# Kernel optimization log

Hardware: AMD Instinct MI355X
Metric: run time of the kernel (lower is better)

The kernel has to match this reference:

```python
import jax, jax.numpy as jnp
import numpy as np

Q = 1024   # num_queries = 32*32
S = 1024   # memory / out seq len
B = 8      # batch
D = 256    # hidden_dim
H = 8      # nhead
FF = 1024  # dim_feedforward (expert hidden)
E = 8      # moe_nume
K = 2      # moe_topk
EPS = 1e-5


def layer_norm(x, g, b):
    mu = jnp.mean(x, axis=-1, keepdims=True)
    var = jnp.var(x, axis=-1, keepdims=True)
    return (x - mu) * jax.lax.rsqrt(var + EPS) * g + b


def mha(q, k, v, wi, bi, wo, bo):
    # q: [Lq,B,D], k/v: [Lk,B,D]; torch nn.MultiheadAttention math (packed in_proj)
    Lq, Bq, Dm = q.shape
    Lk = k.shape[0]
    hd = Dm // H
    wq, wk, wv = jnp.split(wi, 3, axis=0)
    bq, bk, bv = jnp.split(bi, 3)
    qp = (q @ wq.T + bq).reshape(Lq, Bq, H, hd).transpose(1, 2, 0, 3)  # [B,H,Lq,hd]
    kp = (k @ wk.T + bk).reshape(Lk, Bq, H, hd).transpose(1, 2, 0, 3)  # [B,H,Lk,hd]
    vp = (v @ wv.T + bv).reshape(Lk, Bq, H, hd).transpose(1, 2, 0, 3)
    scores = jnp.einsum('bhqd,bhkd->bhqk', qp, kp) / jnp.sqrt(jnp.asarray(hd, q.dtype))
    attn = jax.nn.softmax(scores, axis=-1)
    o = jnp.einsum('bhqk,bhkd->bhqd', attn, vp)          # [B,H,Lq,hd]
    o = o.transpose(2, 0, 1, 3).reshape(Lq, Bq, Dm)       # back to [Lq,B,D]
    return o @ wo.T + bo


def moe_ffn(x, gate_w, gate_b, w1, b1, w2, b2):
    # x: [T,D]. NaiveGate: top-k of linear logits, softmax over the k logits.
    logits = x @ gate_w.T + gate_b                        # [T,E]
    vals, idx = jax.lax.top_k(logits, K)                  # [T,K]
    score = jax.nn.softmax(vals, axis=-1)                 # [T,K]
    T = x.shape[0]
    g = jnp.zeros((T, E), x.dtype).at[jnp.arange(T)[:, None], idx].set(score)
    y = jnp.zeros_like(x)
    for e in range(E):  # fixed small expert count
        h = jax.nn.relu(x @ w1[e].T + b1[e])              # [T,FF]
        y = y + g[:, e:e + 1] * (h @ w2[e].T + b2[e])     # [T,D]
    return y


def setup_inputs() -> dict:
    key = jax.random.key(0)
    ks = jax.random.split(key, 24)
    sc = 0.02
    n = lambda i, shp, s=sc: jax.random.normal(ks[i], shp, jnp.float32) * s
    return {
        'out':    jax.random.normal(ks[0], (S, B, D), jnp.float32),
        'memory': jax.random.normal(ks[1], (S, B, D), jnp.float32),
        'embed':  jax.random.normal(ks[2], (Q, D), jnp.float32),
        'sa_wi': n(3, (3 * D, D)), 'sa_bi': jnp.zeros((3 * D,), jnp.float32),
        'sa_wo': n(4, (D, D)),     'sa_bo': jnp.zeros((D,), jnp.float32),
        'ca_wi': n(5, (3 * D, D)), 'ca_bi': jnp.zeros((3 * D,), jnp.float32),
        'ca_wo': n(6, (D, D)),     'ca_bo': jnp.zeros((D,), jnp.float32),
        'n1_g': jnp.ones((D,), jnp.float32), 'n1_b': jnp.zeros((D,), jnp.float32),
        'n2_g': jnp.ones((D,), jnp.float32), 'n2_b': jnp.zeros((D,), jnp.float32),
        'gate_w': n(7, (E, D)), 'gate_b': jnp.zeros((E,), jnp.float32),
        'w1': n(8, (E, FF, D)), 'b1': jnp.zeros((E, FF), jnp.float32),
        'w2': n(9, (E, D, FF)), 'b2': jnp.zeros((E, D), jnp.float32),
    }


def reference(out, memory, embed, sa_wi, sa_bi, sa_wo, sa_bo,
              ca_wi, ca_bi, ca_wo, ca_bo, n1_g, n1_b, n2_g, n2_b,
              gate_w, gate_b, w1, b1, w2, b2):
    # forward_post path (normalize_before=False); pos/masks are None; dropout=eval
    tgt = jnp.broadcast_to(embed[:, None, :], (Q, B, D))
    t2 = mha(tgt, memory, memory, sa_wi, sa_bi, sa_wo, sa_bo)
    tgt = layer_norm(tgt + t2, n1_g, n1_b)
    t2 = mha(tgt, out, out, ca_wi, ca_bi, ca_wo, ca_bo)
    tgt = layer_norm(tgt + t2, n2_g, n2_b)
    # CustomizedMoEPositionwiseFF, pre_lnorm=False: output = inp + moe(inp)
    core = moe_ffn(tgt.reshape(-1, D), gate_w, gate_b, w1, b1, w2, b2).reshape(Q, B, D)
    return tgt + core
```

## Files before the change

### kernel.cpp

```cpp
#include <hip/hip_runtime.h>
#include <hip/hip_bf16.h>


#define DEV static __device__ __forceinline__

typedef __hip_bfloat16 bf16;
typedef __bf16 b8 __attribute__((ext_vector_type(8)));
typedef float fx4 __attribute__((ext_vector_type(4)));

DEV bf16 f2b(float f) { return __float2bfloat16(f); }
DEV float b2f(bf16 h) { return __bfloat162float(h); }

template <int KSTEPS>
DEV void gemm_core(const bf16* __restrict__ A, const int* arow, int lda,
                   const bf16* __restrict__ W, int nbase, int ldb, int lane,
                   fx4 acc[4][4]) {
  const int r = lane & 15, ko = (lane >> 4) * 8;
  const b8* ap[4];
  const b8* bp[4];
#pragma unroll
  for (int i = 0; i < 4; ++i) {
    ap[i] = reinterpret_cast<const b8*>(A + (size_t)arow[i] * lda + ko);
    bp[i] = reinterpret_cast<const b8*>(W + (size_t)(nbase + i * 16 + r) * ldb + ko);
  }
#pragma unroll 4
  for (int ks = 0; ks < KSTEPS; ++ks) {
    b8 a[4], b[4];
#pragma unroll
    for (int i = 0; i < 4; ++i) { a[i] = ap[i][ks * 4]; b[i] = bp[i][ks * 4]; }
#pragma unroll
    for (int i = 0; i < 4; ++i)
#pragma unroll
      for (int j = 0; j < 4; ++j)
        acc[i][j] = __builtin_amdgcn_mfma_f32_16x16x32_bf16(a[i], b[j], acc[i][j], 0, 0, 0);
  }
}

template <int KSTEPS>
DEV void gemm3(const bf16* __restrict__ Ah, const bf16* __restrict__ Al,
               const int* arow, int lda,
               const bf16* __restrict__ Wh, const bf16* __restrict__ Wl,
               int nbase, int ldb, int lane, fx4 acc[4][4]) {
  const int r = lane & 15, ko = (lane >> 4) * 8;
  const b8 *aph[4], *apl[4], *bph[4], *bpl[4];
#pragma unroll
  for (int i = 0; i < 4; ++i) {
    size_t ao = (size_t)arow[i] * lda + ko;
    size_t bo = (size_t)(nbase + i * 16 + r) * ldb + ko;
    aph[i] = reinterpret_cast<const b8*>(Ah + ao);
    apl[i] = reinterpret_cast<const b8*>(Al + ao);
    bph[i] = reinterpret_cast<const b8*>(Wh + bo);
    bpl[i] = reinterpret_cast<const b8*>(Wl + bo);
  }
#pragma unroll 2
  for (int ks = 0; ks < KSTEPS; ++ks) {
    b8 ah[4], al[4], bh[4], bl[4];
#pragma unroll
    for (int i = 0; i < 4; ++i) {
      ah[i] = aph[i][ks * 4]; al[i] = apl[i][ks * 4];
      bh[i] = bph[i][ks * 4]; bl[i] = bpl[i][ks * 4];
    }
#pragma unroll
    for (int i = 0; i < 4; ++i)
#pragma unroll
      for (int j = 0; j < 4; ++j) {
        acc[i][j] = __builtin_amdgcn_mfma_f32_16x16x32_bf16(ah[i], bh[j], acc[i][j], 0, 0, 0);
        acc[i][j] = __builtin_amdgcn_mfma_f32_16x16x32_bf16(ah[i], bl[j], acc[i][j], 0, 0, 0);
        acc[i][j] = __builtin_amdgcn_mfma_f32_16x16x32_bf16(al[i], bh[j], acc[i][j], 0, 0, 0);
      }
  }
}

struct CvtS {
  const float* s[7];
  bf16* dh[7];
  bf16* dl[7];
  int cum[8];
};

__global__ __launch_bounds__(256) void k_cvt_split(CvtS c, int total4) {
  int i = blockIdx.x * 256 + threadIdx.x;
  if (i >= total4) return;
  int idx = i * 4;
#pragma unroll
  for (int seg = 0; seg < 7; ++seg) {
    if (idx < c.cum[seg + 1]) {
      int l = idx - c.cum[seg];
      float4 v = *reinterpret_cast<const float4*>(c.s[seg] + l);
      bf16* dh = c.dh[seg] + l;
      bf16* dl = c.dl[seg] + l;
      float a[4] = {v.x, v.y, v.z, v.w};
#pragma unroll
      for (int t = 0; t < 4; ++t) {
        bf16 h = f2b(a[t]);
        dh[t] = h;
        dl[t] = f2b(a[t] - b2f(h));
      }
      return;
    }
  }
}

struct CvtP {
  const float* s[2];
  bf16* d[2];
  int cum[3];
};

__global__ __launch_bounds__(256) void k_cvt(CvtP c, int total4) {
  int i = blockIdx.x * 256 + threadIdx.x;
  if (i >= total4) return;
  int idx = i * 4;
#pragma unroll
  for (int seg = 0; seg < 2; ++seg) {
    if (idx < c.cum[seg + 1]) {
      int l = idx - c.cum[seg];
      float4 v = *reinterpret_cast<const float4*>(c.s[seg] + l);
      bf16* dp = c.d[seg] + l;
      dp[0] = f2b(v.x); dp[1] = f2b(v.y); dp[2] = f2b(v.z); dp[3] = f2b(v.w);
      return;
    }
  }
}

__global__ __launch_bounds__(256) void k_qproj_s(
    const bf16* __restrict__ Ah, const bf16* __restrict__ Al,
    const bf16* __restrict__ Wh, const bf16* __restrict__ Wl,
    const float* __restrict__ bias,
    bf16* __restrict__ qh, bf16* __restrict__ ql, int isCA) {
  const int w = threadIdx.x >> 6, lane = threadIdx.x & 63;
  const int mbase = blockIdx.x * 128 + (w >> 1) * 64;
  const int nbase = blockIdx.y * 128 + (w & 1) * 64;
  const int r = lane & 15, g4 = lane >> 4;
  int arow[4];
#pragma unroll
  for (int i = 0; i < 4; ++i) arow[i] = mbase + i * 16 + r;
  fx4 acc[4][4] = {};
  gemm3<8>(Ah, Al, arow, 256, Wh, Wl, nbase, 256, lane, acc);
#pragma unroll
  for (int i = 0; i < 4; ++i)
#pragma unroll
    for (int j = 0; j < 4; ++j)
#pragma unroll
      for (int jj = 0; jj < 4; ++jj) {
        int mm = mbase + i * 16 + g4 * 4 + jj;
        int nn = nbase + j * 16 + r;
        float v = (acc[i][j][jj] + bias[nn]) * 0.17677669529663687f;
        int h = nn >> 5, d = nn & 31;
        size_t o;
        if (isCA) o = (((size_t)((mm & 7) * 8 + h)) * 1024 + (mm >> 3)) * 32 + d;
        else      o = ((size_t)h * 1024 + mm) * 32 + d;
        bf16 hv = f2b(v);
        qh[o] = hv;
        ql[o] = f2b(v - b2f(hv));
      }
}

__global__ __launch_bounds__(256) void k_kvproj_s(
    const bf16* __restrict__ Ah, const bf16* __restrict__ Al,
    const bf16* __restrict__ Wh, const bf16* __restrict__ Wl,
    const float* __restrict__ bias,
    bf16* __restrict__ kh, bf16* __restrict__ kl,
    bf16* __restrict__ vh, bf16* __restrict__ vl) {
  const int w = threadIdx.x >> 6, lane = threadIdx.x & 63;
  const int mbase = blockIdx.x * 128 + (w >> 1) * 64;
  const int nbase = blockIdx.y * 128 + (w & 1) * 64;
  const int r = lane & 15, g4 = lane >> 4;
  int arow[4];
#pragma unroll
  for (int i = 0; i < 4; ++i) arow[i] = mbase + i * 16 + r;
  fx4 acc[4][4] = {};
  gemm3<8>(Ah, Al, arow, 256, Wh, Wl, nbase, 256, lane, acc);
#pragma unroll
  for (int i = 0; i < 4; ++i)
#pragma unroll
    for (int j = 0; j < 4; ++j)
#pragma unroll
      for (int jj = 0; jj < 4; ++jj) {
        int mm = mbase + i * 16 + g4 * 4 + jj;
        int nn = nbase + j * 16 + r;
        float v = acc[i][j][jj] + bias[nn];
        int s = mm >> 3, bb = mm & 7;
        int hh = (nn & 255) >> 5, d = nn & 31;
        bf16 hv = f2b(v);
        bf16 lv = f2b(v - b2f(hv));
        if (nn < 256) {
          size_t o = (((size_t)(bb * 8 + hh)) * 1024 + s) * 32 + d;
          kh[o] = hv; kl[o] = lv;
        } else {
          size_t o = (((size_t)(bb * 8 + hh)) * 32 + d) * 1024 + s;
          vh[o] = hv; vl[o] = lv;
        }
      }
}

__global__ __launch_bounds__(256, 4) void k_attn_s(
    const bf16* __restrict__ qth, const bf16* __restrict__ qtl,
    const bf16* __restrict__ kth, const bf16* __restrict__ ktl,
    const bf16* __restrict__ vth, const bf16* __restrict__ vtl,
    bf16* __restrict__ aoh, bf16* __restrict__ aol, int caFlag) {
  __shared__ __align__(16) char smem[18432];
  bf16 (*Ph)[16][72] = reinterpret_cast<bf16 (*)[16][72]>(smem);
  bf16 (*Pl)[16][72] = reinterpret_cast<bf16 (*)[16][72]>(smem + 9216);
  float (*Cb)[64][16] = reinterpret_cast<float (*)[64][16]>(smem);
  const int w = threadIdx.x >> 6, lane = threadIdx.x & 63;
  const int n = blockIdx.y * 32 + blockIdx.x;
  const int c = n & 7, rem = n >> 3;
  const int xt = rem & 31, a = rem >> 5;
  const int bh = a * 8 + c;
  const int b = bh >> 3, h = bh & 7;
  const int q0 = xt * 32 + (w >> 1) * 16;
  const int sbase = (w & 1) * 512;
  const int r = lane & 15, ko = (lane >> 4) * 8, g4 = lane >> 4;
  const size_t qoff = (size_t)(caFlag ? bh : h) * 1024 * 32;
  const size_t koff = (size_t)bh * 1024 * 32;
  const size_t voff = (size_t)bh * 32 * 1024;
  const b8 qfh = *reinterpret_cast<const b8*>(qth + qoff + (size_t)(q0 + r) * 32 + ko);
  const b8 qfl = *reinterpret_cast<const b8*>(qtl + qoff + (size_t)(q0 + r) * 32 + ko);
  fx4 o0 = {}, o1 = {};
  const fx4 zz = {};
  float lr[4] = {0.f, 0.f, 0.f, 0.f};
  for (int it = 0; it < 8; ++it) {
    const int s0 = sbase + it * 64;
    fx4 sf[4];
#pragma unroll
    for (int kb4 = 0; kb4 < 4; ++kb4) {
      size_t o = koff + (size_t)(s0 + kb4 * 16 + r) * 32 + ko;
      b8 kfh = *reinterpret_cast<const b8*>(kth + o);
      b8 kfl = *reinterpret_cast<const b8*>(ktl + o);
      fx4 t = __builtin_amdgcn_mfma_f32_16x16x32_bf16(qfl, kfh, zz, 0, 0, 0);
      t = __builtin_amdgcn_mfma_f32_16x16x32_bf16(qfh, kfl, t, 0, 0, 0);
      sf[kb4] = __builtin_amdgcn_mfma_f32_16x16x32_bf16(qfh, kfh, t, 0, 0, 0);
    }
#pragma unroll
    for (int kb4 = 0; kb4 < 4; ++kb4)
#pragma unroll
      for (int j = 0; j < 4; ++j) {
        float p = __expf(sf[kb4][j]);
        sf[kb4][j] = p;
        lr[j] += p;
        bf16 ph = f2b(p);
        Ph[w][g4 * 4 + j][kb4 * 16 + r] = ph;
        Pl[w][g4 * 4 + j][kb4 * 16 + r] = f2b(p - b2f(ph));
      }
    asm volatile("s_waitcnt lgkmcnt(0)" ::: "memory");
    b8 pa0h = *reinterpret_cast<const b8*>(&Ph[w][r][ko]);
    b8 pa1h = *reinterpret_cast<const b8*>(&Ph[w][r][32 + ko]);
    b8 pa0l = *reinterpret_cast<const b8*>(&Pl[w][r][ko]);
    b8 pa1l = *reinterpret_cast<const b8*>(&Pl[w][r][32 + ko]);
#pragma unroll
    for (int db = 0; db < 2; ++db) {
      size_t o0a = voff + (size_t)(db * 16 + r) * 1024 + s0 + ko;
      b8 v0h = *reinterpret_cast<const b8*>(vth + o0a);
      b8 v0l = *reinterpret_cast<const b8*>(vtl + o0a);
      b8 v1h = *reinterpret_cast<const b8*>(vth + o0a + 32);
      b8 v1l = *reinterpret_cast<const b8*>(vtl + o0a + 32);
      fx4& oo = db ? o1 : o0;
      oo = __builtin_amdgcn_mfma_f32_16x16x32_bf16(pa0h, v0h, oo, 0, 0, 0);
      oo = __builtin_amdgcn_mfma_f32_16x16x32_bf16(pa0h, v0l, oo, 0, 0, 0);
      oo = __builtin_amdgcn_mfma_f32_16x16x32_bf16(pa0l, v0h, oo, 0, 0, 0);
      oo = __builtin_amdgcn_mfma_f32_16x16x32_bf16(pa1h, v1h, oo, 0, 0, 0);
      oo = __builtin_amdgcn_mfma_f32_16x16x32_bf16(pa1h, v1l, oo, 0, 0, 0);
      oo = __builtin_amdgcn_mfma_f32_16x16x32_bf16(pa1l, v1h, oo, 0, 0, 0);
    }
  }
#pragma unroll
  for (int j = 0; j < 4; ++j) {
    lr[j] += __shfl_xor(lr[j], 1);
    lr[j] += __shfl_xor(lr[j], 2);
    lr[j] += __shfl_xor(lr[j], 4);
    lr[j] += __shfl_xor(lr[j], 8);
  }
  __syncthreads();
  {
    float* cw = &Cb[w][lane][0];
#pragma unroll
    for (int j = 0; j < 4; ++j) {
      cw[j] = lr[j]; cw[4 + j] = o0[j]; cw[8 + j] = o1[j];
    }
  }
  __syncthreads();
  if ((w & 1) == 0) {
    const float* cp = &Cb[w ^ 1][lane][0];
#pragma unroll
    for (int j = 0; j < 4; ++j) {
      float inv = 1.f / (lr[j] + cp[j]);
      float a0 = (o0[j] + cp[4 + j]) * inv;
      float a1 = (o1[j] + cp[8 + j]) * inv;
      int q = q0 + g4 * 4 + j;
      size_t rowoff = ((size_t)q * 8 + b) * 256 + h * 32;
      bf16 h0 = f2b(a0), h1 = f2b(a1);
      aoh[rowoff + r] = h0;      aol[rowoff + r] = f2b(a0 - b2f(h0));
      aoh[rowoff + 16 + r] = h1; aol[rowoff + 16 + r] = f2b(a1 - b2f(h1));
    }
  }
}

__global__ __launch_bounds__(256) void k_oproj_s(
    const bf16* __restrict__ Ah, const bf16* __restrict__ Al,
    const bf16* __restrict__ Wh, const bf16* __restrict__ Wl,
    const float* __restrict__ bias, const float* __restrict__ res,
    int resBroadcast, float* __restrict__ yo) {
  const int w = threadIdx.x >> 6, lane = threadIdx.x & 63;
  const int mbase = blockIdx.x * 128 + (w >> 1) * 64;
  const int nbase = blockIdx.y * 128 + (w & 1) * 64;
  const int r = lane & 15, g4 = lane >> 4;
  int arow[4];
#pragma unroll
  for (int i = 0; i < 4; ++i) arow[i] = mbase + i * 16 + r;
  fx4 acc[4][4] = {};
  gemm3<8>(Ah, Al, arow, 256, Wh, Wl, nbase, 256, lane, acc);
#pragma unroll
  for (int i = 0; i < 4; ++i)
#pragma unroll
    for (int j = 0; j < 4; ++j)
#pragma unroll
      for (int jj = 0; jj < 4; ++jj) {
        int mm = mbase + i * 16 + g4 * 4 + jj;
        int nn = nbase + j * 16 + r;
        size_t roff = resBroadcast ? (size_t)(mm >> 3) * 256 : (size_t)mm * 256;
        yo[(size_t)mm * 256 + nn] = acc[i][j][jj] + bias[nn] + res[roff + nn];
      }
}

__global__ __launch_bounds__(256) void k_ln(const float* __restrict__ y,
                                            const float* __restrict__ g,
                                            const float* __restrict__ bta,
                                            float* __restrict__ of,
                                            bf16* __restrict__ obh,
                                            bf16* __restrict__ obl) {
  const int row = blockIdx.x * 4 + (threadIdx.x >> 6);
  const int lane = threadIdx.x & 63;
  float4 x = reinterpret_cast<const float4*>(y + (size_t)row * 256)[lane];
  float s1 = x.x + x.y + x.z + x.w;
  float s2 = x.x * x.x + x.y * x.y + x.z * x.z + x.w * x.w;
#pragma unroll
  for (int m = 1; m < 64; m <<= 1) {
    s1 += __shfl_xor(s1, m);
    s2 += __shfl_xor(s2, m);
  }
  float mean = s1 * (1.0f / 256.0f);
  float var = s2 * (1.0f / 256.0f) - mean * mean;
  float rs = 1.0f / sqrtf(var + 1e-5f);
  float4 gv = reinterpret_cast<const float4*>(g)[lane];
  float4 bv = reinterpret_cast<const float4*>(bta)[lane];
  float o[4];
  o[0] = (x.x - mean) * rs * gv.x + bv.x;
  o[1] = (x.y - mean) * rs * gv.y + bv.y;
  o[2] = (x.z - mean) * rs * gv.z + bv.z;
  o[3] = (x.w - mean) * rs * gv.w + bv.w;
  float4 ov = {o[0], o[1], o[2], o[3]};
  reinterpret_cast<float4*>(of + (size_t)row * 256)[lane] = ov;
  bf16* dh = obh + (size_t)row * 256 + lane * 4;
  bf16* dl = obl + (size_t)row * 256 + lane * 4;
#pragma unroll
  for (int t = 0; t < 4; ++t) {
    bf16 hv = f2b(o[t]);
    dh[t] = hv;
    dl[t] = f2b(o[t] - b2f(hv));
  }
}

__global__ __launch_bounds__(256) void k_gate(const float* __restrict__ x,
                                              const float* __restrict__ gw,
                                              const float* __restrict__ gb,
                                              int* __restrict__ e0a, int* __restrict__ e1a,
                                              float* __restrict__ w0a, float* __restrict__ w1a) {
  __shared__ float W[2048];
  const int tid = threadIdx.x;
  for (int i = tid; i < 2048; i += 256) W[i] = gw[i];
  __syncthreads();
  const int wv = tid >> 6, lane = tid & 63;
  const int t = blockIdx.x * 4 + wv;
  float4 v = reinterpret_cast<const float4*>(x + (size_t)t * 256)[lane];
  double pe[8];
#pragma unroll
  for (int e = 0; e < 8; ++e) {
    float4 wv4 = reinterpret_cast<const float4*>(&W[e * 256])[lane];
    pe[e] = (double)v.x * wv4.x + (double)v.y * wv4.y +
            (double)v.z * wv4.z + (double)v.w * wv4.w;
  }
#pragma unroll
  for (int e = 0; e < 8; ++e)
#pragma unroll
    for (int m = 1; m < 64; m <<= 1) pe[e] += __shfl_xor(pe[e], m);
  if (lane == 0) {
    float lg[8];
#pragma unroll
    for (int e = 0; e < 8; ++e) lg[e] = (float)(pe[e] + (double)gb[e]);
    int e0 = 0; float v0 = lg[0];
#pragma unroll
    for (int e = 1; e < 8; ++e) if (lg[e] > v0) { v0 = lg[e]; e0 = e; }
    int e1 = -1; float v1 = -1e30f;
#pragma unroll
    for (int e = 0; e < 8; ++e) {
      if (e == e0) continue;
      if (lg[e] > v1) { v1 = lg[e]; e1 = e; }
    }
    float z = __expf(v1 - v0);
    float inv = 1.f / (1.f + z);
    e0a[t] = e0; e1a[t] = e1; w0a[t] = inv; w1a[t] = z * inv;
  }
}

__global__ __launch_bounds__(256) void k_hist(const int* __restrict__ e0a,
                                              const int* __restrict__ e1a,
                                              int* __restrict__ part) {
  __shared__ int lh[4][8];
  const int tid = threadIdx.x, w = tid >> 6;
  const int t = blockIdx.x * 256 + tid;
  const int e0 = e0a[t], e1 = e1a[t];
  int cnt[8];
#pragma unroll
  for (int e = 0; e < 8; ++e) {
    unsigned long long m0 = __ballot(e0 == e);
    unsigned long long m1 = __ballot(e1 == e);
    cnt[e] = __popcll(m0) + __popcll(m1);
  }
  if ((tid & 63) == 0) {
#pragma unroll
    for (int e = 0; e < 8; ++e) lh[w][e] = cnt[e];
  }
  __syncthreads();
  if (tid < 8) part[blockIdx.x * 8 + tid] = lh[0][tid] + lh[1][tid] + lh[2][tid] + lh[3][tid];
}

__global__ void k_scan(const int* __restrict__ part, int* __restrict__ base,
                       int* __restrict__ counts, int* __restrict__ offs) {
  const int lane = threadIdx.x;
  int run = 0;
#pragma unroll
  for (int e = 0; e < 8; ++e) {
    int v = (lane < 32) ? part[lane * 8 + e] : 0;
    int s = v;
#pragma unroll
    for (int off = 1; off < 64; off <<= 1) {
      int u = __shfl_up(s, off);
      if (lane >= off) s += u;
    }
    int tot = __shfl(s, 31);
    if (lane < 32) base[lane * 8 + e] = run + (s - v);
    if (lane == 0) { counts[e] = tot; offs[e] = run; }
    run += tot;
  }
}

__global__ __launch_bounds__(256) void k_scatter(const int* __restrict__ e0a,
                                                 const int* __restrict__ e1a,
                                                 const float* __restrict__ w0a,
                                                 const float* __restrict__ w1a,
                                                 const int* __restrict__ base,
                                                 int* __restrict__ entries,
                                                 float* __restrict__ ew,
                                                 int* __restrict__ slot0,
                                                 int* __restrict__ slot1) {
  __shared__ int cur[8];
  const int tid = threadIdx.x;
  if (tid < 8) cur[tid] = base[blockIdx.x * 8 + tid];
  __syncthreads();
  const int t = blockIdx.x * 256 + tid;
  int e0 = e0a[t];
  int i0 = atomicAdd(&cur[e0], 1);
  entries[i0] = t; ew[i0] = w0a[t]; slot0[t] = i0;
  int e1 = e1a[t];
  int i1 = atomicAdd(&cur[e1], 1);
  entries[i1] = t; ew[i1] = w1a[t]; slot1[t] = i1;
}

__global__ __launch_bounds__(256) void k_ffn1(const bf16* __restrict__ X,
                                              const bf16* __restrict__ w1b,
                                              const float* __restrict__ b1,
                                              const int* __restrict__ entries,
                                              const int* __restrict__ counts,
                                              const int* __restrict__ offs,
                                              bf16* __restrict__ hbuf) {
  const int e = blockIdx.z;
  const int ne = counts[e];
  if ((int)(blockIdx.x * 128) >= ne) return;
  const int base = offs[e];
  const int w = threadIdx.x >> 6, lane = threadIdx.x & 63;
  const int mbase = blockIdx.x * 128 + (w >> 1) * 64;
  const int nbase = blockIdx.y * 128 + (w & 1) * 64;
  const int r = lane & 15, g4 = lane >> 4;
  int arow[4];
#pragma unroll
  for (int i = 0; i < 4; ++i) {
    int mm = mbase + i * 16 + r;
    if (mm > ne - 1) mm = ne - 1;
    arow[i] = entries[base + mm];
  }
  fx4 acc[4][4] = {};
  gemm_core<8>(X, arow, 256, w1b + (size_t)e * 262144, nbase, 256, lane, acc);
  const float* be = b1 + e * 1024;
#pragma unroll
  for (int i = 0; i < 4; ++i)
#pragma unroll
    for (int j = 0; j < 4; ++j)
#pragma unroll
      for (int jj = 0; jj < 4; ++jj) {
        int mm = mbase + i * 16 + g4 * 4 + jj;
        if (mm < ne) {
          int nn = nbase + j * 16 + r;
          float v = fmaxf(acc[i][j][jj] + be[nn], 0.f);
          hbuf[(size_t)(base + mm) * 1024 + nn] = f2b(v);
        }
      }
}

__global__ __launch_bounds__(256) void k_ffn2(const bf16* __restrict__ hbuf,
                                              const bf16* __restrict__ w2b,
                                              const float* __restrict__ b2,
                                              const float* __restrict__ ew,
                                              const int* __restrict__ counts,
                                              const int* __restrict__ offs,
                                              float* __restrict__ ybuf) {
  const int e = blockIdx.z;
  const int ne = counts[e];
  if ((int)(blockIdx.x * 128) >= ne) return;
  const int base = offs[e];
  const int w = threadIdx.x >> 6, lane = threadIdx.x & 63;
  const int mbase = blockIdx.x * 128 + (w >> 1) * 64;
  const int nbase = blockIdx.y * 128 + (w & 1) * 64;
  const int r = lane & 15, g4 = lane >> 4;
  int arow[4];
#pragma unroll
  for (int i = 0; i < 4; ++i) {
    int mm = mbase + i * 16 + r;
    if (mm > ne - 1) mm = ne - 1;
    arow[i] = base + mm;
  }
  fx4 acc[4][4] = {};
  gemm_core<32>(hbuf, arow, 1024, w2b + (size_t)e * 262144, nbase, 1024, lane, acc);
  const float* be = b2 + e * 256;
#pragma unroll
  for (int i = 0; i < 4; ++i)
#pragma unroll
    for (int j = 0; j < 4; ++j)
#pragma unroll
      for (int jj = 0; jj < 4; ++jj) {
        int mm = mbase + i * 16 + g4 * 4 + jj;
        if (mm < ne) {
          int nn = nbase + j * 16 + r;
          int idx = base + mm;
          ybuf[(size_t)idx * 256 + nn] = (acc[i][j][jj] + be[nn]) * ew[idx];
        }
      }
}

__global__ __launch_bounds__(256) void k_final(const float* __restrict__ tgt2,
                                               const float* __restrict__ ybuf,
                                               const int* __restrict__ slot0,
                                               const int* __restrict__ slot1,
                                               float* __restrict__ o) {
  const int w = threadIdx.x >> 6, lane = threadIdx.x & 63;
  const int t = blockIdx.x * 4 + w;
  float4 a = reinterpret_cast<const float4*>(tgt2 + (size_t)t * 256)[lane];
  float4 y0 = reinterpret_cast<const float4*>(ybuf + (size_t)slot0[t] * 256)[lane];
  float4 y1 = reinterpret_cast<const float4*>(ybuf + (size_t)slot1[t] * 256)[lane];
  float4 z;
  z.x = a.x + y0.x + y1.x;
  z.y = a.y + y0.y + y1.y;
  z.z = a.z + y0.z + y1.z;
  z.w = a.w + y0.w + y1.w;
  reinterpret_cast<float4*>(o + (size_t)t * 256)[lane] = z;
}

extern "C" void kernel_launch(void* const* d_in, const int* in_sizes, int n_in,
                              void* d_out, int out_size, void* d_ws, size_t ws_size,
                              hipStream_t stream) {
  const float* in_out   = (const float*)d_in[0];
  const float* in_mem   = (const float*)d_in[1];
  const float* in_embed = (const float*)d_in[2];
  const float* sa_wi = (const float*)d_in[3];
  const float* sa_bi = (const float*)d_in[4];
  const float* sa_wo = (const float*)d_in[5];
  const float* sa_bo = (const float*)d_in[6];
  const float* ca_wi = (const float*)d_in[7];
  const float* ca_bi = (const float*)d_in[8];
  const float* ca_wo = (const float*)d_in[9];
  const float* ca_bo = (const float*)d_in[10];
  const float* n1g = (const float*)d_in[11];
  const float* n1b = (const float*)d_in[12];
  const float* n2g = (const float*)d_in[13];
  const float* n2b = (const float*)d_in[14];
  const float* gw = (const float*)d_in[15];
  const float* gb = (const float*)d_in[16];
  const float* w1 = (const float*)d_in[17];
  const float* b1 = (const float*)d_in[18];
  const float* w2 = (const float*)d_in[19];
  const float* b2 = (const float*)d_in[20];
  (void)in_sizes; (void)n_in; (void)out_size; (void)ws_size;

  char* p = (char*)d_ws;
  auto alloc = [&](size_t bytes) -> char* {
    char* q = p;
    p += (bytes + 511) & ~(size_t)511;
    return q;
  };
  bf16* sa_wi_h = (bf16*)alloc(196608 * 2); bf16* sa_wi_l = (bf16*)alloc(196608 * 2);
  bf16* ca_wi_h = (bf16*)alloc(196608 * 2); bf16* ca_wi_l = (bf16*)alloc(196608 * 2);
  bf16* sa_wo_h = (bf16*)alloc(65536 * 2);  bf16* sa_wo_l = (bf16*)alloc(65536 * 2);
  bf16* ca_wo_h = (bf16*)alloc(65536 * 2);  bf16* ca_wo_l = (bf16*)alloc(65536 * 2);
  bf16* w1_b    = (bf16*)alloc(2097152 * 2);
  bf16* w2_b    = (bf16*)alloc(2097152 * 2);
  bf16* embed_h = (bf16*)alloc(262144 * 2); bf16* embed_l = (bf16*)alloc(262144 * 2);
  bf16* mem_h   = (bf16*)alloc(2097152 * 2); bf16* mem_l  = (bf16*)alloc(2097152 * 2);
  bf16* out_h   = (bf16*)alloc(2097152 * 2); bf16* out_l  = (bf16*)alloc(2097152 * 2);
  bf16* q_sa_h  = (bf16*)alloc(262144 * 2);  bf16* q_sa_l = (bf16*)alloc(262144 * 2);
  bf16* k_h     = (bf16*)alloc(2097152 * 2); bf16* k_l    = (bf16*)alloc(2097152 * 2);
  bf16* v_h     = (bf16*)alloc(2097152 * 2); bf16* v_l    = (bf16*)alloc(2097152 * 2);
  bf16* attn_h  = (bf16*)alloc(2097152 * 2); bf16* attn_l = (bf16*)alloc(2097152 * 2);
  bf16* q_ca_h  = (bf16*)alloc(2097152 * 2); bf16* q_ca_l = (bf16*)alloc(2097152 * 2);
  float* y      = (float*)alloc(2097152 * 4);
  float* tgt1_f = (float*)alloc(2097152 * 4);
  bf16* tgt1_h  = (bf16*)alloc(2097152 * 2); bf16* tgt1_l = (bf16*)alloc(2097152 * 2);
  float* tgt2_f = (float*)alloc(2097152 * 4);
  bf16* tgt2_h  = (bf16*)alloc(2097152 * 2); bf16* tgt2_l = (bf16*)alloc(2097152 * 2);
  bf16* hbuf    = (bf16*)alloc((size_t)16384 * 1024 * 2);
  int* e0a      = (int*)alloc(8192 * 4);
  int* e1a      = (int*)alloc(8192 * 4);
  float* w0a    = (float*)alloc(8192 * 4);
  float* w1a    = (float*)alloc(8192 * 4);
  int* entries  = (int*)alloc(16384 * 4);
  float* ewt    = (float*)alloc(16384 * 4);
  int* slot0    = (int*)alloc(8192 * 4);
  int* slot1    = (int*)alloc(8192 * 4);
  int* part     = (int*)alloc(32 * 8 * 4);
  int* basep    = (int*)alloc(32 * 8 * 4);
  int* ctrl     = (int*)alloc(64);
  int* counts = ctrl;
  int* offs = ctrl + 8;
  float* ybuf = (float*)attn_h;

  CvtS cs{};
  cs.s[0] = sa_wi;    cs.dh[0] = sa_wi_h; cs.dl[0] = sa_wi_l;
  cs.s[1] = ca_wi;    cs.dh[1] = ca_wi_h; cs.dl[1] = ca_wi_l;
  cs.s[2] = sa_wo;    cs.dh[2] = sa_wo_h; cs.dl[2] = sa_wo_l;
  cs.s[3] = ca_wo;    cs.dh[3] = ca_wo_h; cs.dl[3] = ca_wo_l;
  cs.s[4] = in_embed; cs.dh[4] = embed_h; cs.dl[4] = embed_l;
  cs.s[5] = in_mem;   cs.dh[5] = mem_h;   cs.dl[5] = mem_l;
  cs.s[6] = in_out;   cs.dh[6] = out_h;   cs.dl[6] = out_l;
  int cumS[8] = {0, 196608, 393216, 458752, 524288, 786432, 2883584, 4980736};
  for (int i = 0; i < 8; ++i) cs.cum[i] = cumS[i];
  k_cvt_split<<<4864, 256, 0, stream>>>(cs, 1245184);

  CvtP cp{};
  cp.s[0] = w1; cp.d[0] = w1_b;
  cp.s[1] = w2; cp.d[1] = w2_b;
  cp.cum[0] = 0; cp.cum[1] = 2097152; cp.cum[2] = 4194304;
  k_cvt<<<4096, 256, 0, stream>>>(cp, 1048576);

  k_qproj_s<<<dim3(8, 2), 256, 0, stream>>>(embed_h, embed_l, sa_wi_h, sa_wi_l,
                                            sa_bi, q_sa_h, q_sa_l, 0);
  k_kvproj_s<<<dim3(64, 4), 256, 0, stream>>>(mem_h, mem_l, sa_wi_h + 65536,
                                              sa_wi_l + 65536, sa_bi + 256,
                                              k_h, k_l, v_h, v_l);
  k_attn_s<<<dim3(32, 64), 256, 0, stream>>>(q_sa_h, q_sa_l, k_h, k_l, v_h, v_l,
                                             attn_h, attn_l, 0);
  k_oproj_s<<<dim3(64, 2), 256, 0, stream>>>(attn_h, attn_l, sa_wo_h, sa_wo_l,
                                             sa_bo, in_embed, 1, y);
  k_ln<<<2048, 256, 0, stream>>>(y, n1g, n1b, tgt1_f, tgt1_h, tgt1_l);

  k_qproj_s<<<dim3(64, 2), 256, 0, stream>>>(tgt1_h, tgt1_l, ca_wi_h, ca_wi_l,
                                             ca_bi, q_ca_h, q_ca_l, 1);
  k_kvproj_s<<<dim3(64, 4), 256, 0, stream>>>(out_h, out_l, ca_wi_h + 65536,
                                              ca_wi_l + 65536, ca_bi + 256,
                                              k_h, k_l, v_h, v_l);
  k_attn_s<<<dim3(32, 64), 256, 0, stream>>>(q_ca_h, q_ca_l, k_h, k_l, v_h, v_l,
                                             attn_h, attn_l, 1);
  k_oproj_s<<<dim3(64, 2), 256, 0, stream>>>(attn_h, attn_l, ca_wo_h, ca_wo_l,
                                             ca_bo, tgt1_f, 0, y);
  k_ln<<<2048, 256, 0, stream>>>(y, n2g, n2b, tgt2_f, tgt2_h, tgt2_l);

  k_gate<<<2048, 256, 0, stream>>>(tgt2_f, gw, gb, e0a, e1a, w0a, w1a);
  k_hist<<<32, 256, 0, stream>>>(e0a, e1a, part);
  k_scan<<<1, 64, 0, stream>>>(part, basep, counts, offs);
  k_scatter<<<32, 256, 0, stream>>>(e0a, e1a, w0a, w1a, basep, entries, ewt, slot0, slot1);
  k_ffn1<<<dim3(128, 8, 8), 256, 0, stream>>>(tgt2_h, w1_b, b1, entries, counts, offs, hbuf);
  k_ffn2<<<dim3(128, 2, 8), 256, 0, stream>>>(hbuf, w2_b, b2, ewt, counts, offs, ybuf);
  k_final<<<2048, 256, 0, stream>>>(tgt2_f, ybuf, slot0, slot1, (float*)d_out);
}
```

Measured before the change: 687.3 us.

## Compute transposed QK scores so P feeds PV MFMA directly from registers

Swaps the operands of the QK^T MFMA so each lane holds a column of scores laid out the way the PV MFMA's A operand expects. The softmax probabilities then feed 16x16x16 bf16 MFMAs straight from registers, with no round trip through shared memory and no waitcnt barrier per tile. Row sums become a two-step cross-lane shuffle plus a per-row broadcast at the end. In exchange, the PV step uses twice as many smaller-K MFMA instructions and narrower 8-byte V loads.

```diff
diff --git a/kernel.cpp b/kernel.cpp
--- a/kernel.cpp
+++ b/kernel.cpp
@@ -6,10 +6,25 @@
 
 typedef __hip_bfloat16 bf16;
 typedef __bf16 b8 __attribute__((ext_vector_type(8)));
+typedef __bf16 b4 __attribute__((ext_vector_type(4)));
+typedef short s4 __attribute__((ext_vector_type(4)));
 typedef float fx4 __attribute__((ext_vector_type(4)));
 
 DEV bf16 f2b(float f) { return __float2bfloat16(f); }
 DEV float b2f(bf16 h) { return __bfloat162float(h); }
+
+DEV fx4 mfma16(b4 a, b4 b, fx4 c) {
+#if __has_builtin(__builtin_amdgcn_mfma_f32_16x16x16_bf16)
+  return __builtin_amdgcn_mfma_f32_16x16x16_bf16(a, b, c, 0, 0, 0);
+#elif __has_builtin(__builtin_amdgcn_mfma_f32_16x16x16bf16_1k)
+  s4 as = __builtin_bit_cast(s4, a);
+  s4 bs = __builtin_bit_cast(s4, b);
+  return __builtin_amdgcn_mfma_f32_16x16x16bf16_1k(as, bs, c, 0, 0, 0);
+#else
+  asm("v_mfma_f32_16x16x16_bf16 %0, %1, %2, %0" : "+v"(c) : "v"(a), "v"(b));
+  return c;
+#endif
+}
 
 template <int KSTEPS>
 DEV void gemm_core(const bf16* __restrict__ A, const int* arow, int lda,
@@ -199,95 +214,78 @@
     const bf16* __restrict__ kth, const bf16* __restrict__ ktl,
     const bf16* __restrict__ vth, const bf16* __restrict__ vtl,
     bf16* __restrict__ aoh, bf16* __restrict__ aol, int caFlag) {
-  __shared__ __align__(16) char smem[18432];
-  bf16 (*Ph)[16][72] = reinterpret_cast<bf16 (*)[16][72]>(smem);
-  bf16 (*Pl)[16][72] = reinterpret_cast<bf16 (*)[16][72]>(smem + 9216);
-  float (*Cb)[64][16] = reinterpret_cast<float (*)[64][16]>(smem);
+  __shared__ float Cb[4][64][12];
   const int w = threadIdx.x >> 6, lane = threadIdx.x & 63;
   const int n = blockIdx.y * 32 + blockIdx.x;
-  const int c = n & 7, rem = n >> 3;
+  const int cx = n & 7, rem = n >> 3;
   const int xt = rem & 31, a = rem >> 5;
-  const int bh = a * 8 + c;
+  const int bh = a * 8 + cx;
   const int b = bh >> 3, h = bh & 7;
   const int q0 = xt * 32 + (w >> 1) * 16;
   const int sbase = (w & 1) * 512;
-  const int r = lane & 15, ko = (lane >> 4) * 8, g4 = lane >> 4;
-  const size_t qoff = (size_t)(caFlag ? bh : h) * 1024 * 32;
-  const size_t koff = (size_t)bh * 1024 * 32;
-  const size_t voff = (size_t)bh * 32 * 1024;
+  const int r = lane & 15, g4 = lane >> 4, ko = g4 * 8;
+  const size_t qoff = (size_t)(caFlag ? bh : h) * 32768;
+  const size_t koff = (size_t)bh * 32768;
+  const size_t voff = (size_t)bh * 32768;
   const b8 qfh = *reinterpret_cast<const b8*>(qth + qoff + (size_t)(q0 + r) * 32 + ko);
   const b8 qfl = *reinterpret_cast<const b8*>(qtl + qoff + (size_t)(q0 + r) * 32 + ko);
   fx4 o0 = {}, o1 = {};
   const fx4 zz = {};
-  float lr[4] = {0.f, 0.f, 0.f, 0.f};
+  float lsum = 0.f;
   for (int it = 0; it < 8; ++it) {
     const int s0 = sbase + it * 64;
-    fx4 sf[4];
 #pragma unroll
     for (int kb4 = 0; kb4 < 4; ++kb4) {
-      size_t o = koff + (size_t)(s0 + kb4 * 16 + r) * 32 + ko;
+      const int st = s0 + kb4 * 16;
+      size_t o = koff + (size_t)(st + r) * 32 + ko;
       b8 kfh = *reinterpret_cast<const b8*>(kth + o);
       b8 kfl = *reinterpret_cast<const b8*>(ktl + o);
-      fx4 t = __builtin_amdgcn_mfma_f32_16x16x32_bf16(qfl, kfh, zz, 0, 0, 0);
-      t = __builtin_amdgcn_mfma_f32_16x16x32_bf16(qfh, kfl, t, 0, 0, 0);
-      sf[kb4] = __builtin_amdgcn_mfma_f32_16x16x32_bf16(qfh, kfh, t, 0, 0, 0);
+      fx4 t = __builtin_amdgcn_mfma_f32_16x16x32_bf16(kfh, qfl, zz, 0, 0, 0);
+      t = __builtin_amdgcn_mfma_f32_16x16x32_bf16(kfl, qfh, t, 0, 0, 0);
+      fx4 sf = __builtin_amdgcn_mfma_f32_16x16x32_bf16(kfh, qfh, t, 0, 0, 0);
+      b4 ph, pl;
+#pragma unroll
+      for (int j = 0; j < 4; ++j) {
+        float p = __expf(sf[j]);
+        lsum += p;
+        __bf16 hv = (__bf16)p;
+        ph[j] = hv;
+        pl[j] = (__bf16)(p - (float)hv);
+      }
+      const bf16* vb = vth + voff + (size_t)st + g4 * 4;
+      const bf16* vbl = vtl + voff + (size_t)st + g4 * 4;
+#pragma unroll
+      for (int db = 0; db < 2; ++db) {
+        size_t vo = (size_t)(db * 16 + r) * 1024;
+        b4 v_h = *reinterpret_cast<const b4*>(vb + vo);
+        b4 v_l = *reinterpret_cast<const b4*>(vbl + vo);
+        fx4& oo = db ? o1 : o0;
+        oo = mfma16(ph, v_h, oo);
+        oo = mfma16(ph, v_l, oo);
+        oo = mfma16(pl, v_h, oo);
+      }
     }
-#pragma unroll
-    for (int kb4 = 0; kb4 < 4; ++kb4)
-#pragma unroll
-      for (int j = 0; j < 4; ++j) {
-        float p = __expf(sf[kb4][j]);
-        sf[kb4][j] = p;
-        lr[j] += p;
-        bf16 ph = f2b(p);
-        Ph[w][g4 * 4 + j][kb4 * 16 + r] = ph;
-        Pl[w][g4 * 4 + j][kb4 * 16 + r] = f2b(p - b2f(ph));
-      }
-    asm volatile("s_waitcnt lgkmcnt(0)" ::: "memory");
-    b8 pa0h = *reinterpret_cast<const b8*>(&Ph[w][r][ko]);
-    b8 pa1h = *reinterpret_cast<const b8*>(&Ph[w][r][32 + ko]);
-    b8 pa0l = *reinterpret_cast<const b8*>(&Pl[w][r][ko]);
-    b8 pa1l = *reinterpret_cast<const b8*>(&Pl[w][r][32 + ko]);
-#pragma unroll
-    for (int db = 0; db < 2; ++db) {
-      size_t o0a = voff + (size_t)(db * 16 + r) * 1024 + s0 + ko;
-      b8 v0h = *reinterpret_cast<const b8*>(vth + o0a);
-      b8 v0l = *reinterpret_cast<const b8*>(vtl + o0a);
-      b8 v1h = *reinterpret_cast<const b8*>(vth + o0a + 32);
-      b8 v1l = *reinterpret_cast<const b8*>(vtl + o0a + 32);
-      fx4& oo = db ? o1 : o0;
-      oo = __builtin_amdgcn_mfma_f32_16x16x32_bf16(pa0h, v0h, oo, 0, 0, 0);
-      oo = __builtin_amdgcn_mfma_f32_16x16x32_bf16(pa0h, v0l, oo, 0, 0, 0);
-      oo = __builtin_amdgcn_mfma_f32_16x16x32_bf16(pa0l, v0h, oo, 0, 0, 0);
-      oo = __builtin_amdgcn_mfma_f32_16x16x32_bf16(pa1h, v1h, oo, 0, 0, 0);
-      oo = __builtin_amdgcn_mfma_f32_16x16x32_bf16(pa1h, v1l, oo, 0, 0, 0);
-      oo = __builtin_amdgcn_mfma_f32_16x16x32_bf16(pa1l, v1h, oo, 0, 0, 0);
-    }
-  }
-#pragma unroll
-  for (int j = 0; j < 4; ++j) {
-    lr[j] += __shfl_xor(lr[j], 1);
-    lr[j] += __shfl_xor(lr[j], 2);
-    lr[j] += __shfl_xor(lr[j], 4);
-    lr[j] += __shfl_xor(lr[j], 8);
-  }
+  }
+  lsum += __shfl_xor(lsum, 16);
+  lsum += __shfl_xor(lsum, 32);
   __syncthreads();
   {
     float* cw = &Cb[w][lane][0];
-#pragma unroll
-    for (int j = 0; j < 4; ++j) {
-      cw[j] = lr[j]; cw[4 + j] = o0[j]; cw[8 + j] = o1[j];
-    }
+    cw[0] = lsum;
+#pragma unroll
+    for (int j = 0; j < 4; ++j) { cw[1 + j] = o0[j]; cw[5 + j] = o1[j]; }
   }
   __syncthreads();
   if ((w & 1) == 0) {
     const float* cp = &Cb[w ^ 1][lane][0];
+    float lt = lsum + cp[0];
 #pragma unroll
     for (int j = 0; j < 4; ++j) {
-      float inv = 1.f / (lr[j] + cp[j]);
-      float a0 = (o0[j] + cp[4 + j]) * inv;
-      float a1 = (o1[j] + cp[8 + j]) * inv;
-      int q = q0 + g4 * 4 + j;
+      float lrow = __shfl(lt, 4 * g4 + j);
+      float inv = 1.f / lrow;
+      float a0 = (o0[j] + cp[1 + j]) * inv;
+      float a1 = (o1[j] + cp[5 + j]) * inv;
+      int q = q0 + 4 * g4 + j;
       size_t rowoff = ((size_t)q * 8 + b) * 256 + h * 32;
       bf16 h0 = f2b(a0), h1 = f2b(a1);
       aoh[rowoff + r] = h0;      aol[rowoff + r] = f2b(a0 - b2f(h0));
```

After: 815.7 us. 1.19x slower.
